# Kernel optimization log

Measured on AMD Instinct MI355X. Metric: run time of the kernel, lower is better.

## Reference

```python
import jax, jax.numpy as jnp
import numpy as np

B, N, T, F, H, O = 32, 256, 64, 16, 128, 1  # batch, nodes, seq_len, input, hidden, output


def setup_inputs() -> dict:
    key = jax.random.key(0)
    ks = jax.random.split(key, 14)
    s = 0.05
    nrm = lambda k, shp: jax.random.normal(k, shp, jnp.float32) * s
    return {
        "x": jax.random.normal(ks[0], (B, N, T, F), jnp.float32),
        "A": jax.random.normal(ks[1], (N, N), jnp.float32),
        "W_ih0": nrm(ks[2], (4 * H, F)),
        "W_hh0": nrm(ks[3], (4 * H, H)),
        "b_ih0": nrm(ks[4], (4 * H,)),
        "b_hh0": nrm(ks[5], (4 * H,)),
        "W_ih1": nrm(ks[6], (4 * H, H)),
        "W_hh1": nrm(ks[7], (4 * H, H)),
        "b_ih1": nrm(ks[8], (4 * H,)),
        "b_hh1": nrm(ks[9], (4 * H,)),
        "W1": nrm(ks[10], (H, H)),
        "W2": nrm(ks[11], (H, H)),
        "W3": nrm(ks[12], (H, H)),
        "Wfc": nrm(ks[13], (O, H)),
    }


def _lstm_layer(inp, W_ih, W_hh, b_ih, b_hh):
    # inp: (BN, T, F_in). PyTorch LSTM gate order: i, f, g, o.
    BN = inp.shape[0]
    Hd = W_hh.shape[1]
    h0 = jnp.zeros((BN, Hd), inp.dtype)
    c0 = jnp.zeros((BN, Hd), inp.dtype)

    def step(carry, x_t):
        h, c = carry
        g = x_t @ W_ih.T + b_ih + h @ W_hh.T + b_hh
        i, f, gg, o = jnp.split(g, 4, axis=-1)
        c = jax.nn.sigmoid(f) * c + jax.nn.sigmoid(i) * jnp.tanh(gg)
        h = jax.nn.sigmoid(o) * jnp.tanh(c)
        return (h, c), h

    (hT, _), hs = jax.lax.scan(step, (h0, c0), jnp.swapaxes(inp, 0, 1))
    return jnp.swapaxes(hs, 0, 1), hT  # (BN, T, H), (BN, H)


def reference(x, A, W_ih0, W_hh0, b_ih0, b_hh0, W_ih1, W_hh1, b_ih1, b_hh1, W1, W2, W3, Wfc):
    Bx, Nx, Tx, Fx = x.shape
    # Batch the per-node LSTM calls: all (batch, node) pairs share LSTM weights.
    xs = x.reshape(Bx * Nx, Tx, Fx)
    h1_seq, _ = _lstm_layer(xs, W_ih0, W_hh0, b_ih0, b_hh0)
    _, hT = _lstm_layer(h1_seq, W_ih1, W_hh1, b_ih1, b_hh1)  # last layer final hidden
    h_LSTM = hT.reshape(Bx, Nx, -1).transpose(0, 2, 1)  # (B, H, N)

    A_p = jax.nn.sigmoid(A)
    HA = jnp.einsum('bhn,nl->bhl', h_LSTM, A_p)        # H @ A'
    h_A = HA.transpose(0, 2, 1)                        # (B, N, H)
    W1hA = jnp.einsum('bnh,gh->bgn', h_A, W1)          # (B, H, N)
    mid = jax.nn.relu(jnp.einsum('bnh,gh->bng', h_A, W2))
    W3r = jnp.einsum('bng,fg->bfn', mid, W3)           # (B, H, N)
    ATW = jnp.einsum('bhn,nl->bhl', W3r, A_p)
    alpha = 0.9
    h_out = (1.0 - alpha) * ATW + alpha * W1hA         # (B, H, N)
    # Per-node MLP (shared weights) + sigmoid, batched over nodes.
    out = jax.nn.sigmoid(jnp.einsum('bhn,oh->bno', h_out, Wfc))  # (B, N, O)
    return out
```

## Files before the change

### kernel.cpp

```cpp
#include <hip/hip_runtime.h>


typedef __attribute__((ext_vector_type(4))) float f32x4;
typedef __attribute__((ext_vector_type(2))) float f32x2;
typedef __attribute__((ext_vector_type(8))) __bf16 bf16x8;
typedef __attribute__((ext_vector_type(8))) unsigned short u16x8;
typedef __attribute__((ext_vector_type(4))) unsigned short u16x4;

#define DEV static __device__ __forceinline__

DEV unsigned short f2bf(float f) {
  unsigned u = __builtin_bit_cast(unsigned, f);
  u = u + 0x7fffu + ((u >> 16) & 1u);
  return (unsigned short)(u >> 16);
}
DEV float bf2f(unsigned short s) {
  unsigned u = ((unsigned)s) << 16;
  return __builtin_bit_cast(float, u);
}

DEV float fexp2(float x) { return __builtin_amdgcn_exp2f(x); }
DEV f32x2 exp2v2(f32x2 x) { f32x2 r; r[0] = fexp2(x[0]); r[1] = fexp2(x[1]); return r; }
DEV f32x2 rcpv2(f32x2 x) {
  f32x2 r; r[0] = __builtin_amdgcn_rcpf(x[0]); r[1] = __builtin_amdgcn_rcpf(x[1]); return r;
}

DEV unsigned cell_pair(f32x2 gi, f32x2 gf, f32x2 gg, f32x2 go, f32x2& cs) {
  const float K2 = 2.88539008f;
  f32x2 one = {1.f, 1.f};
  f32x2 t1 = exp2v2(gg);
  f32x2 t2 = exp2v2((f32x2){-gi[0], -gi[1]});
  f32x2 ef = exp2v2((f32x2){-gf[0], -gf[1]});
  f32x2 d1 = t1 + one;
  f32x2 den1 = d1 * t2 + d1;
  f32x2 it = (t1 - one) * rcpv2(den1);
  cs = rcpv2(one + ef) * cs + (f32x2){K2 * it[0], K2 * it[1]};
  f32x2 t3 = exp2v2(cs);
  f32x2 t4 = exp2v2((f32x2){-go[0], -go[1]});
  f32x2 d3 = t3 + one;
  f32x2 den3 = d3 * t4 + d3;
  f32x2 h = (t3 - one) * rcpv2(den3);
  unsigned r;
  asm("v_cvt_pk_bf16_f32 %0, %1, %2" : "=v"(r) : "v"(h[0]), "v"(h[1]));
  return r;
}

#define O_W0PK   0
#define O_W1PK   163840
#define O_APK    425984
#define O_W1APK  557056
#define O_W2APK  589824
#define O_W3APK  622592
#define O_BIAS0  655360
#define O_BIAS1  657408
#define O_HTT    659456
#define O_HAT    2756608
#define O_MIDT   4853760
#define O_W1HAT  6950912
#define O_W3R    9048064
#define O_XPK    11145216
#define O_H1     44699648

#define PREP_TOT 328704

DEV int gr_unit(int rtg, int lql) { return 16 * (rtg >> 2) + 4 * lql + (rtg & 3); }

__global__ void prep_kernel(const float* __restrict__ A,
    const float* __restrict__ Wih0, const float* __restrict__ Whh0,
    const float* __restrict__ bih0, const float* __restrict__ bhh0,
    const float* __restrict__ Wih1, const float* __restrict__ Whh1,
    const float* __restrict__ bih1, const float* __restrict__ bhh1,
    const float* __restrict__ W1, const float* __restrict__ W2,
    const float* __restrict__ W3, char* __restrict__ ws)
{
  const float K1 = 1.44269504f, K2 = 2.88539008f;
  int idx = blockIdx.x * blockDim.x + threadIdx.x;
  if (idx >= PREP_TOT) return;
  if (idx < 81920) {
    int o = idx, i = o & 7, l = (o >> 3) & 63, f = o >> 9;
    int kt = f % 5, rtg = f / 5;
    int lr = l & 15, lq = l >> 4;
    int p = lr & 3, lql = (lr >> 2) & 3;
    int gc = p * 128 + gr_unit(rtg, lql);
    float sc = (p == 2) ? K2 : K1;
    float v;
    if (kt < 4) v = Whh0[gc * 128 + 32 * kt + 8 * lq + i];
    else {
      int kk = 8 * lq + i;
      v = (kk < 16) ? Wih0[gc * 16 + kk]
                    : (kk == 16 ? (bih0[gc] + bhh0[gc]) : 0.f);
    }
    ((unsigned short*)(ws + O_W0PK))[idx] = f2bf(v * sc);
  } else if (idx < 212992) {
    int o = idx - 81920, i = o & 7, l = (o >> 3) & 63, f = o >> 9;
    int kt = f & 7, rtg = f >> 3;
    int lr = l & 15, lq = l >> 4;
    int p = lr & 3, lql = (lr >> 2) & 3;
    int gc = p * 128 + gr_unit(rtg, lql);
    float sc = (p == 2) ? K2 : K1;
    float v = (kt < 4) ? Wih1[gc * 128 + 32 * kt + 8 * lq + i]
                       : Whh1[gc * 128 + 32 * (kt - 4) + 8 * lq + i];
    ((unsigned short*)(ws + O_W1PK))[o] = f2bf(v * sc);
  } else if (idx < 278528) {
    int o = idx - 212992, i = o & 7, l = (o >> 3) & 63, f = o >> 9;
    int kt = f & 7, ct = f >> 3;
    int n = 32 * kt + 8 * (l >> 4) + i;
    int lc = 16 * ct + (l & 15);
    float e = fexp2(-K1 * A[n * 256 + lc]);
    ((unsigned short*)(ws + O_APK))[o] = f2bf(__builtin_amdgcn_rcpf(1.f + e));
  } else if (idx < 327680) {
    int o = idx - 278528;
    int m = o >> 14;
    int oo = o & 16383;
    int i = oo & 7, l = (oo >> 3) & 63, f = oo >> 9;
    int kt = f & 3, rt = f >> 2;
    int g = 16 * rt + (l & 15);
    int k = 32 * kt + 8 * (l >> 4) + i;
    const float* W = (m == 0) ? W1 : (m == 1) ? W2 : W3;
    unsigned short* dst = (unsigned short*)(ws + ((m == 0) ? O_W1APK : (m == 1) ? O_W2APK : O_W3APK));
    dst[oo] = f2bf(W[g * 128 + k]);
  } else if (idx < 328192) {
    int c = idx - 327680;
    ((float*)(ws + O_BIAS0))[c] = bih0[c] + bhh0[c];
  } else {
    int c = idx - 328192;
    float sc = ((c >> 7) == 2) ? K2 : K1;
    ((float*)(ws + O_BIAS1))[c] = (bih1[c] + bhh1[c]) * sc;
  }
}

__global__ void prepx_kernel(const float* __restrict__ x, char* __restrict__ ws)
{
  int tid = blockIdx.x * 256 + threadIdx.x;
  int dat = (tid < 1048576) ? 1 : 0;
  int id = tid & 1048575;
  int half = id & 1, t = (id >> 1) & 63, row = id >> 7;
  u16x8 v = (u16x8)0;
  if (dat) {
    const float* p = x + ((long)row * 64 + t) * 16 + 8 * half;
    float4 a = *(const float4*)p;
    float4 b = *(const float4*)(p + 4);
    v[0] = f2bf(a.x); v[1] = f2bf(a.y); v[2] = f2bf(a.z); v[3] = f2bf(a.w);
    v[4] = f2bf(b.x); v[5] = f2bf(b.y); v[6] = f2bf(b.z); v[7] = f2bf(b.w);
  } else if (half == 0) {
    v[0] = 0x3F80;
  }
  int lane = (dat ? 0 : 32) + half * 16 + (row & 15);
  int rt = row >> 4;
  ((u16x8*)(ws + O_XPK))[(rt * 64 + t) * 64 + lane] = v;
}

__global__ __launch_bounds__(512, 2) void lstm0_k(char* __restrict__ ws, int row_base)
{
  const unsigned short* W0pk = (const unsigned short*)(ws + O_W0PK);
  const unsigned short* xpk = (const unsigned short*)(ws + O_XPK);
  unsigned short* h1 = (unsigned short*)(ws + O_H1);

  int tid = threadIdx.x;
  int Wv = tid >> 6, l = tid & 63, lr = l & 15, lq = l >> 4;
  int lrow = blockIdx.x * 16;
  long grow0 = (long)row_base + lrow;

  __shared__ unsigned char hlds[2][4096];
  ((unsigned long long*)hlds[0])[tid] = 0ull;

  bf16x8 Af[4][5];
#pragma unroll
  for (int rt = 0; rt < 4; rt++)
#pragma unroll
    for (int kt = 0; kt < 5; kt++)
      Af[rt][kt] = ((const bf16x8*)W0pk)[((4 * Wv + rt) * 5 + kt) * 64 + l];

  f32x2 cs01 = {0.f, 0.f}, cs23 = {0.f, 0.f};

  int rd[4];
#pragma unroll
  for (int kt = 0; kt < 4; kt++)
    rd[kt] = lr * 256 + ((64 * kt + 16 * lq) ^ ((lr & 7) << 4));
  int whp = lr * 256 + ((32 * Wv + 8 * lq) ^ ((lr & 7) << 4));

  int pr = tid >> 5, pc2 = tid & 31;
  int sld = pr * 256 + ((8 * pc2) ^ ((pr & 7) << 4));
  unsigned short* st = h1 + (long)(lrow + pr) * 8192 + 4 * pc2;

  const bf16x8* xp = (const bf16x8*)xpk + (grow0 >> 4) * 4096 + l;
  bf16x8 xb = xp[0];
  __syncthreads();

  for (int t = 0; t < 64; t++) {
    const unsigned char* rbuf = hlds[t & 1];
    unsigned char* wbuf = hlds[(t & 1) ^ 1];
    int tn = (t < 63) ? t + 1 : 63;
    bf16x8 xbn = xp[tn * 64];

    f32x4 acc[4];
#pragma unroll
    for (int rt = 0; rt < 4; rt++) acc[rt] = (f32x4){0.f, 0.f, 0.f, 0.f};
#pragma unroll
    for (int kt = 0; kt < 4; kt++) {
      bf16x8 hb = *(const bf16x8*)(rbuf + rd[kt]);
#pragma unroll
      for (int rt = 0; rt < 4; rt++)
        acc[rt] = __builtin_amdgcn_mfma_f32_16x16x32_bf16(Af[rt][kt], hb, acc[rt], 0, 0, 0);
    }
#pragma unroll
    for (int rt = 0; rt < 4; rt++)
      acc[rt] = __builtin_amdgcn_mfma_f32_16x16x32_bf16(Af[rt][4], xb, acc[rt], 0, 0, 0);

    unsigned pk01 = cell_pair((f32x2){acc[0][0], acc[1][0]}, (f32x2){acc[0][1], acc[1][1]},
                              (f32x2){acc[0][2], acc[1][2]}, (f32x2){acc[0][3], acc[1][3]}, cs01);
    unsigned pk23 = cell_pair((f32x2){acc[2][0], acc[3][0]}, (f32x2){acc[2][1], acc[3][1]},
                              (f32x2){acc[2][2], acc[3][2]}, (f32x2){acc[2][3], acc[3][3]}, cs23);
    unsigned long long pk = ((unsigned long long)pk23 << 32) | pk01;
    *(unsigned long long*)(wbuf + whp) = pk;
    xb = xbn;
    __syncthreads();
    *(unsigned long long*)(st + t * 128) =
        *(const unsigned long long*)(hlds[(t & 1) ^ 1] + sld);
  }
}

__global__ __launch_bounds__(512, 2) void lstm1_k(char* __restrict__ ws, int row_base)
{
  const unsigned short* W1pk = (const unsigned short*)(ws + O_W1PK);
  const float* bias1 = (const float*)(ws + O_BIAS1);
  const unsigned short* h1 = (const unsigned short*)(ws + O_H1);
  unsigned short* hTt = (unsigned short*)(ws + O_HTT);

  int tid = threadIdx.x;
  int Wv = tid >> 6, l = tid & 63, lr = l & 15, lq = l >> 4;
  int lrow = blockIdx.x * 16;
  long grow0 = (long)row_base + lrow;

  __shared__ unsigned char hlds[2][4096];
  __shared__ unsigned char h1s[2][4096];
  ((unsigned long long*)hlds[0])[tid] = 0ull;

  int prow = tid >> 5, pc2 = tid & 31;
  const unsigned short* s0 = h1 + (long)(lrow + prow) * 8192 + 4 * pc2;
  int d0 = prow * 256 + ((8 * pc2) ^ ((prow & 7) << 4));
  *(unsigned long long*)(h1s[0] + d0) = *(const unsigned long long*)s0;

  bf16x8 Af[4][8];
#pragma unroll
  for (int rt = 0; rt < 4; rt++)
#pragma unroll
    for (int kt = 0; kt < 8; kt++)
      Af[rt][kt] = ((const bf16x8*)W1pk)[((4 * Wv + rt) * 8 + kt) * 64 + l];

  f32x4 bias_c[4];
#pragma unroll
  for (int rt = 0; rt < 4; rt++)
#pragma unroll
    for (int r = 0; r < 4; r++)
      bias_c[rt][r] = bias1[r * 128 + 16 * Wv + 4 * lq + rt];

  f32x2 cs01 = {0.f, 0.f}, cs23 = {0.f, 0.f};

  int rd[4];
#pragma unroll
  for (int kt = 0; kt < 4; kt++)
    rd[kt] = lr * 256 + ((64 * kt + 16 * lq) ^ ((lr & 7) << 4));
  int whp = lr * 256 + ((32 * Wv + 8 * lq) ^ ((lr & 7) << 4));
  __syncthreads();

  for (int t = 0; t < 64; t++) {
    const unsigned char* rbuf = hlds[t & 1];
    unsigned char* wbuf = hlds[(t & 1) ^ 1];
    const unsigned char* h1r = h1s[t & 1];
    unsigned char* h1w = h1s[(t & 1) ^ 1];
    int tn = (t < 63) ? t + 1 : 63;
    unsigned long long pf = *(const unsigned long long*)(s0 + tn * 128);

    f32x4 acc[4];
#pragma unroll
    for (int rt = 0; rt < 4; rt++) acc[rt] = bias_c[rt];
#pragma unroll
    for (int kt = 0; kt < 4; kt++) {
      bf16x8 xb = *(const bf16x8*)(h1r + rd[kt]);
#pragma unroll
      for (int rt = 0; rt < 4; rt++)
        acc[rt] = __builtin_amdgcn_mfma_f32_16x16x32_bf16(Af[rt][kt], xb, acc[rt], 0, 0, 0);
    }
#pragma unroll
    for (int kt = 0; kt < 4; kt++) {
      bf16x8 hb = *(const bf16x8*)(rbuf + rd[kt]);
#pragma unroll
      for (int rt = 0; rt < 4; rt++)
        acc[rt] = __builtin_amdgcn_mfma_f32_16x16x32_bf16(Af[rt][4 + kt], hb, acc[rt], 0, 0, 0);
    }
    unsigned pk01 = cell_pair((f32x2){acc[0][0], acc[1][0]}, (f32x2){acc[0][1], acc[1][1]},
                              (f32x2){acc[0][2], acc[1][2]}, (f32x2){acc[0][3], acc[1][3]}, cs01);
    unsigned pk23 = cell_pair((f32x2){acc[2][0], acc[3][0]}, (f32x2){acc[2][1], acc[3][1]},
                              (f32x2){acc[2][2], acc[3][2]}, (f32x2){acc[2][3], acc[3][3]}, cs23);
    *(unsigned long long*)(wbuf + whp) = ((unsigned long long)pk23 << 32) | pk01;
    *(unsigned long long*)(h1w + d0) = pf;
    __syncthreads();
  }

  {
    unsigned long long hp = *(const unsigned long long*)(hlds[0] + whp);
    long grow = grow0 + lr;
    long base = ((grow >> 8) * 128) * 256 + (grow & 255);
    int u0 = 16 * Wv + 4 * lq;
#pragma unroll
    for (int j = 0; j < 4; j++)
      hTt[base + (long)(u0 + j) * 256] = (unsigned short)((hp >> (16 * j)) & 0xffff);
  }
}

__global__ __launch_bounds__(256, 2) void g1_kernel(char* __restrict__ ws)
{
  const unsigned short* hTt = (const unsigned short*)(ws + O_HTT);
  const unsigned short* Apk = (const unsigned short*)(ws + O_APK);
  unsigned short* HAt = (unsigned short*)(ws + O_HAT);
  int tid = threadIdx.x, w = tid >> 6, l = tid & 63, lr = l & 15, lq = l >> 4;
  int bi = blockIdx.x;
  int b = bi >> 3, rtp = (bi >> 1) & 3, ch = bi & 1;
  f32x4 acc[2][2];
#pragma unroll
  for (int i = 0; i < 2; i++)
#pragma unroll
    for (int j = 0; j < 2; j++) acc[i][j] = (f32x4){0.f, 0.f, 0.f, 0.f};
  for (int kt = 0; kt < 8; kt++) {
    bf16x8 af[2];
#pragma unroll
    for (int rtl = 0; rtl < 2; rtl++) {
      int rt = rtp * 2 + rtl;
      af[rtl] = *(const bf16x8*)(hTt + (long)(b * 128 + 16 * rt + lr) * 256 + 32 * kt + 8 * lq);
    }
#pragma unroll
    for (int cti = 0; cti < 2; cti++) {
      int ct = w * 4 + ch * 2 + cti;
      bf16x8 bf = ((const bf16x8*)Apk)[(ct * 8 + kt) * 64 + l];
#pragma unroll
      for (int rtl = 0; rtl < 2; rtl++)
        acc[rtl][cti] = __builtin_amdgcn_mfma_f32_16x16x32_bf16(af[rtl], bf, acc[rtl][cti], 0, 0, 0);
    }
  }
#pragma unroll
  for (int rtl = 0; rtl < 2; rtl++)
#pragma unroll
    for (int cti = 0; cti < 2; cti++) {
      int rt = rtp * 2 + rtl, ct = w * 4 + ch * 2 + cti;
      u16x4 pk;
#pragma unroll
      for (int r = 0; r < 4; r++) pk[r] = f2bf(acc[rtl][cti][r]);
      *(u16x4*)(HAt + (long)(b * 256 + 16 * ct + lr) * 128 + 16 * rt + 4 * lq) = pk;
    }
}

__global__ __launch_bounds__(256, 2) void g2_kernel(char* __restrict__ ws)
{
  const unsigned short* HAt = (const unsigned short*)(ws + O_HAT);
  const unsigned short* W1apk = (const unsigned short*)(ws + O_W1APK);
  const unsigned short* W2apk = (const unsigned short*)(ws + O_W2APK);
  unsigned short* W1hAt = (unsigned short*)(ws + O_W1HAT);
  unsigned short* midT = (unsigned short*)(ws + O_MIDT);
  int tid = threadIdx.x, w = tid >> 6, l = tid & 63, lr = l & 15, lq = l >> 4;
  int bi = blockIdx.x;
  int b = bi >> 3, rtp = (bi >> 1) & 3, ch = bi & 1;
  f32x4 a1[2][2], a2[2][2];
#pragma unroll
  for (int i = 0; i < 2; i++)
#pragma unroll
    for (int j = 0; j < 2; j++) { a1[i][j] = (f32x4){0.f,0.f,0.f,0.f}; a2[i][j] = (f32x4){0.f,0.f,0.f,0.f}; }
  for (int kt = 0; kt < 4; kt++) {
    bf16x8 af1[2], af2[2];
#pragma unroll
    for (int rtl = 0; rtl < 2; rtl++) {
      int rt = rtp * 2 + rtl;
      af1[rtl] = ((const bf16x8*)W1apk)[(rt * 4 + kt) * 64 + l];
      af2[rtl] = ((const bf16x8*)W2apk)[(rt * 4 + kt) * 64 + l];
    }
#pragma unroll
    for (int cti = 0; cti < 2; cti++) {
      int ct = w * 4 + ch * 2 + cti;
      bf16x8 bf = *(const bf16x8*)(HAt + (long)(b * 256 + 16 * ct + lr) * 128 + 32 * kt + 8 * lq);
#pragma unroll
      for (int rtl = 0; rtl < 2; rtl++) {
        a1[rtl][cti] = __builtin_amdgcn_mfma_f32_16x16x32_bf16(af1[rtl], bf, a1[rtl][cti], 0, 0, 0);
        a2[rtl][cti] = __builtin_amdgcn_mfma_f32_16x16x32_bf16(af2[rtl], bf, a2[rtl][cti], 0, 0, 0);
      }
    }
  }
#pragma unroll
  for (int rtl = 0; rtl < 2; rtl++)
#pragma unroll
    for (int cti = 0; cti < 2; cti++) {
      int rt = rtp * 2 + rtl, ct = w * 4 + ch * 2 + cti;
      u16x4 p1, p2;
#pragma unroll
      for (int r = 0; r < 4; r++) {
        p1[r] = f2bf(a1[rtl][cti][r]);
        p2[r] = f2bf(fmaxf(a2[rtl][cti][r], 0.f));
      }
      long off = (long)(b * 256 + 16 * ct + lr) * 128 + 16 * rt + 4 * lq;
      *(u16x4*)(W1hAt + off) = p1;
      *(u16x4*)(midT + off) = p2;
    }
}

__global__ __launch_bounds__(256, 2) void g3_kernel(char* __restrict__ ws)
{
  const unsigned short* midT = (const unsigned short*)(ws + O_MIDT);
  const unsigned short* W3apk = (const unsigned short*)(ws + O_W3APK);
  unsigned short* W3r = (unsigned short*)(ws + O_W3R);
  int tid = threadIdx.x, w = tid >> 6, l = tid & 63, lr = l & 15, lq = l >> 4;
  int bi = blockIdx.x;
  int b = bi >> 3, rtp = (bi >> 1) & 3, ch = bi & 1;
  f32x4 acc[2][2];
#pragma unroll
  for (int i = 0; i < 2; i++)
#pragma unroll
    for (int j = 0; j < 2; j++) acc[i][j] = (f32x4){0.f, 0.f, 0.f, 0.f};
  for (int kt = 0; kt < 4; kt++) {
    bf16x8 af[2];
#pragma unroll
    for (int rtl = 0; rtl < 2; rtl++)
      af[rtl] = ((const bf16x8*)W3apk)[((rtp * 2 + rtl) * 4 + kt) * 64 + l];
#pragma unroll
    for (int cti = 0; cti < 2; cti++) {
      int ct = w * 4 + ch * 2 + cti;
      bf16x8 bf = *(const bf16x8*)(midT + (long)(b * 256 + 16 * ct + lr) * 128 + 32 * kt + 8 * lq);
#pragma unroll
      for (int rtl = 0; rtl < 2; rtl++)
        acc[rtl][cti] = __builtin_amdgcn_mfma_f32_16x16x32_bf16(af[rtl], bf, acc[rtl][cti], 0, 0, 0);
    }
  }
#pragma unroll
  for (int rtl = 0; rtl < 2; rtl++)
#pragma unroll
    for (int cti = 0; cti < 2; cti++) {
      int rt = rtp * 2 + rtl, ct = w * 4 + ch * 2 + cti;
#pragma unroll
      for (int r = 0; r < 4; r++)
        W3r[(long)(b * 128 + 16 * rt + 4 * lq + r) * 256 + 16 * ct + lr] = f2bf(acc[rtl][cti][r]);
    }
}

__global__ __launch_bounds__(256, 2) void g4_kernel(char* __restrict__ ws,
    const float* __restrict__ Wfc, float* __restrict__ out)
{
  const unsigned short* W3r = (const unsigned short*)(ws + O_W3R);
  const unsigned short* Apk = (const unsigned short*)(ws + O_APK);
  const unsigned short* W1hAt = (const unsigned short*)(ws + O_W1HAT);
  int tid = threadIdx.x, w = tid >> 6, l = tid & 63, lr = l & 15, lq = l >> 4;
  int bi = blockIdx.x;
  int b = bi >> 2, cq = bi & 3;
  int ct = cq * 4 + w;
  f32x4 acc[8];
#pragma unroll
  for (int i = 0; i < 8; i++) acc[i] = (f32x4){0.f, 0.f, 0.f, 0.f};
  for (int kt = 0; kt < 8; kt++) {
    bf16x8 bfv = ((const bf16x8*)Apk)[(ct * 8 + kt) * 64 + l];
#pragma unroll
    for (int rt = 0; rt < 8; rt++) {
      bf16x8 af = *(const bf16x8*)(W3r + (long)(b * 128 + 16 * rt + lr) * 256 + 32 * kt + 8 * lq);
      acc[rt] = __builtin_amdgcn_mfma_f32_16x16x32_bf16(af, bfv, acc[rt], 0, 0, 0);
    }
  }
  float psum = 0.f;
#pragma unroll
  for (int rt = 0; rt < 8; rt++) {
    float4 wf = *(const float4*)(Wfc + 16 * rt + 4 * lq);
    u16x4 wv = *(const u16x4*)(W1hAt + (long)(b * 256 + 16 * ct + lr) * 128 + 16 * rt + 4 * lq);
    psum += wf.x * (0.1f * acc[rt][0] + 0.9f * bf2f(wv[0]));
    psum += wf.y * (0.1f * acc[rt][1] + 0.9f * bf2f(wv[1]));
    psum += wf.z * (0.1f * acc[rt][2] + 0.9f * bf2f(wv[2]));
    psum += wf.w * (0.1f * acc[rt][3] + 0.9f * bf2f(wv[3]));
  }
  psum += __shfl_xor(psum, 16);
  psum += __shfl_xor(psum, 32);
  if (lq == 0) out[b * 256 + ct * 16 + lr] = __builtin_amdgcn_rcpf(1.f + fexp2(-1.44269504f * psum));
}

extern "C" void kernel_launch(void* const* d_in, const int* in_sizes, int n_in,
                              void* d_out, int out_size, void* d_ws, size_t ws_size,
                              hipStream_t stream)
{
  const float* x    = (const float*)d_in[0];
  const float* A    = (const float*)d_in[1];
  const float* Wih0 = (const float*)d_in[2];
  const float* Whh0 = (const float*)d_in[3];
  const float* bih0 = (const float*)d_in[4];
  const float* bhh0 = (const float*)d_in[5];
  const float* Wih1 = (const float*)d_in[6];
  const float* Whh1 = (const float*)d_in[7];
  const float* bih1 = (const float*)d_in[8];
  const float* bhh1 = (const float*)d_in[9];
  const float* W1   = (const float*)d_in[10];
  const float* W2   = (const float*)d_in[11];
  const float* W3   = (const float*)d_in[12];
  const float* Wfc  = (const float*)d_in[13];
  char* ws = (char*)d_ws;

  prep_kernel<<<(PREP_TOT + 255) / 256, 256, 0, stream>>>(
      A, Wih0, Whh0, bih0, bhh0, Wih1, Whh1, bih1, bhh1, W1, W2, W3, ws);
  prepx_kernel<<<8192, 256, 0, stream>>>(x, ws);

  size_t need_full = (size_t)O_H1 + 134217728u;
  size_t need_half = (size_t)O_H1 + 67108864u;
  if (ws_size >= need_full) {
    lstm0_k<<<512, 512, 0, stream>>>(ws, 0);
    lstm1_k<<<512, 512, 0, stream>>>(ws, 0);
  } else if (ws_size >= need_half) {
    for (int c = 0; c < 2; c++) {
      lstm0_k<<<256, 512, 0, stream>>>(ws, c * 4096);
      lstm1_k<<<256, 512, 0, stream>>>(ws, c * 4096);
    }
  } else {
    for (int c = 0; c < 4; c++) {
      lstm0_k<<<128, 512, 0, stream>>>(ws, c * 2048);
      lstm1_k<<<128, 512, 0, stream>>>(ws, c * 2048);
    }
  }

  g1_kernel<<<256, 256, 0, stream>>>(ws);
  g2_kernel<<<256, 256, 0, stream>>>(ws);
  g3_kernel<<<256, 256, 0, stream>>>(ws);
  g4_kernel<<<128, 256, 0, stream>>>(ws, Wfc, (float*)d_out);
}
```

Measured before the change: 269.8 us.

## Switch LSTM recurrence to 32x32x16 MFMA with 32-row blocks of 1024 threads

Both LSTM kernels move from 16x16x32 MFMAs with four row tiles per wave to a single 32x32x16 MFMA accumulator per wave. Each block now handles 32 sequence rows with 16 waves, so weights, LDS layouts, swizzles and the x packing are reorganised to match. s_setprio is raised around the MFMA chain. The aim is fewer MFMA issues and more rows per block, at the cost of larger LDS buffers and a larger block, which may limit occupancy under launch_bounds(1024,4).

```diff
diff --git a/kernel.cpp b/kernel.cpp
--- a/kernel.cpp
+++ b/kernel.cpp
@@ -2,6 +2,7 @@
 
 
 typedef __attribute__((ext_vector_type(4))) float f32x4;
+typedef __attribute__((ext_vector_type(16))) float f32x16;
 typedef __attribute__((ext_vector_type(2))) float f32x2;
 typedef __attribute__((ext_vector_type(8))) __bf16 bf16x8;
 typedef __attribute__((ext_vector_type(8))) unsigned short u16x8;
@@ -63,8 +64,6 @@
 
 #define PREP_TOT 328704
 
-DEV int gr_unit(int rtg, int lql) { return 16 * (rtg >> 2) + 4 * lql + (rtg & 3); }
-
 __global__ void prep_kernel(const float* __restrict__ A,
     const float* __restrict__ Wih0, const float* __restrict__ Whh0,
     const float* __restrict__ bih0, const float* __restrict__ bhh0,
@@ -78,28 +77,29 @@
   if (idx >= PREP_TOT) return;
   if (idx < 81920) {
     int o = idx, i = o & 7, l = (o >> 3) & 63, f = o >> 9;
-    int kt = f % 5, rtg = f / 5;
-    int lr = l & 15, lq = l >> 4;
-    int p = lr & 3, lql = (lr >> 2) & 3;
-    int gc = p * 128 + gr_unit(rtg, lql);
+    int kt = f % 10, W = f / 10;
+    int rho = l & 31, hik = l >> 5;
+    int p = rho & 3, hi = (rho >> 2) & 1, q = rho >> 3;
+    int gc = p * 128 + 8 * W + 4 * hi + q;
     float sc = (p == 2) ? K2 : K1;
+    int k = 16 * kt + 8 * hik + i;
     float v;
-    if (kt < 4) v = Whh0[gc * 128 + 32 * kt + 8 * lq + i];
+    if (k < 128) v = Whh0[gc * 128 + k];
     else {
-      int kk = 8 * lq + i;
+      int kk = k - 128;
       v = (kk < 16) ? Wih0[gc * 16 + kk]
                     : (kk == 16 ? (bih0[gc] + bhh0[gc]) : 0.f);
     }
     ((unsigned short*)(ws + O_W0PK))[idx] = f2bf(v * sc);
   } else if (idx < 212992) {
     int o = idx - 81920, i = o & 7, l = (o >> 3) & 63, f = o >> 9;
-    int kt = f & 7, rtg = f >> 3;
-    int lr = l & 15, lq = l >> 4;
-    int p = lr & 3, lql = (lr >> 2) & 3;
-    int gc = p * 128 + gr_unit(rtg, lql);
+    int kt = f & 15, W = f >> 4;
+    int rho = l & 31, hik = l >> 5;
+    int p = rho & 3, hi = (rho >> 2) & 1, q = rho >> 3;
+    int gc = p * 128 + 8 * W + 4 * hi + q;
     float sc = (p == 2) ? K2 : K1;
-    float v = (kt < 4) ? Wih1[gc * 128 + 32 * kt + 8 * lq + i]
-                       : Whh1[gc * 128 + 32 * (kt - 4) + 8 * lq + i];
+    int k = 16 * kt + 8 * hik + i;
+    float v = (k < 128) ? Wih1[gc * 128 + k] : Whh1[gc * 128 + (k - 128)];
     ((unsigned short*)(ws + O_W1PK))[o] = f2bf(v * sc);
   } else if (idx < 278528) {
     int o = idx - 212992, i = o & 7, l = (o >> 3) & 63, f = o >> 9;
@@ -132,95 +132,92 @@
 __global__ void prepx_kernel(const float* __restrict__ x, char* __restrict__ ws)
 {
   int tid = blockIdx.x * 256 + threadIdx.x;
-  int dat = (tid < 1048576) ? 1 : 0;
-  int id = tid & 1048575;
-  int half = id & 1, t = (id >> 1) & 63, row = id >> 7;
+  int lane = tid & 63;
+  int slice = (tid >> 6) & 1;
+  int t = (tid >> 7) & 63;
+  int rt32 = tid >> 13;
+  int col = lane & 31, hi = lane >> 5;
   u16x8 v = (u16x8)0;
-  if (dat) {
-    const float* p = x + ((long)row * 64 + t) * 16 + 8 * half;
+  if (slice == 0) {
+    const float* p = x + ((long)(rt32 * 32 + col) * 64 + t) * 16 + 8 * hi;
     float4 a = *(const float4*)p;
     float4 b = *(const float4*)(p + 4);
     v[0] = f2bf(a.x); v[1] = f2bf(a.y); v[2] = f2bf(a.z); v[3] = f2bf(a.w);
     v[4] = f2bf(b.x); v[5] = f2bf(b.y); v[6] = f2bf(b.z); v[7] = f2bf(b.w);
-  } else if (half == 0) {
+  } else if (hi == 0) {
     v[0] = 0x3F80;
   }
-  int lane = (dat ? 0 : 32) + half * 16 + (row & 15);
-  int rt = row >> 4;
-  ((u16x8*)(ws + O_XPK))[(rt * 64 + t) * 64 + lane] = v;
-}
-
-__global__ __launch_bounds__(512, 2) void lstm0_k(char* __restrict__ ws, int row_base)
+  ((u16x8*)(ws + O_XPK))[tid] = v;
+}
+
+__global__ __launch_bounds__(1024, 4) void lstm0_k(char* __restrict__ ws, int row_base)
 {
   const unsigned short* W0pk = (const unsigned short*)(ws + O_W0PK);
   const unsigned short* xpk = (const unsigned short*)(ws + O_XPK);
   unsigned short* h1 = (unsigned short*)(ws + O_H1);
 
   int tid = threadIdx.x;
-  int Wv = tid >> 6, l = tid & 63, lr = l & 15, lq = l >> 4;
-  int lrow = blockIdx.x * 16;
+  int Wv = tid >> 6, l = tid & 63, col = l & 31, hi = l >> 5;
+  int lrow = blockIdx.x * 32;
   long grow0 = (long)row_base + lrow;
 
-  __shared__ unsigned char hlds[2][4096];
+  __shared__ unsigned char hlds[2][8192];
   ((unsigned long long*)hlds[0])[tid] = 0ull;
 
-  bf16x8 Af[4][5];
-#pragma unroll
-  for (int rt = 0; rt < 4; rt++)
-#pragma unroll
-    for (int kt = 0; kt < 5; kt++)
-      Af[rt][kt] = ((const bf16x8*)W0pk)[((4 * Wv + rt) * 5 + kt) * 64 + l];
+  bf16x8 Af[10];
+#pragma unroll
+  for (int kt = 0; kt < 10; kt++)
+    Af[kt] = ((const bf16x8*)W0pk)[(Wv * 10 + kt) * 64 + l];
 
   f32x2 cs01 = {0.f, 0.f}, cs23 = {0.f, 0.f};
 
-  int rd[4];
-#pragma unroll
-  for (int kt = 0; kt < 4; kt++)
-    rd[kt] = lr * 256 + ((64 * kt + 16 * lq) ^ ((lr & 7) << 4));
-  int whp = lr * 256 + ((32 * Wv + 8 * lq) ^ ((lr & 7) << 4));
-
-  int pr = tid >> 5, pc2 = tid & 31;
-  int sld = pr * 256 + ((8 * pc2) ^ ((pr & 7) << 4));
-  unsigned short* st = h1 + (long)(lrow + pr) * 8192 + 4 * pc2;
-
-  const bf16x8* xp = (const bf16x8*)xpk + (grow0 >> 4) * 4096 + l;
-  bf16x8 xb = xp[0];
+  int rd[8];
+#pragma unroll
+  for (int ks = 0; ks < 8; ks++)
+    rd[ks] = col * 256 + ((32 * ks + 16 * hi) ^ ((col & 15) << 4));
+  int whp = col * 256 + ((16 * Wv + 8 * hi) ^ ((col & 15) << 4));
+
+  int pr = tid >> 5, pc8 = tid & 31;
+  int sld = pr * 256 + ((8 * pc8) ^ ((pr & 15) << 4));
+  unsigned short* st = h1 + (long)(lrow + pr) * 8192 + 4 * pc8;
+
+  long xbase = (grow0 >> 5) * 8192 + l;
+  const bf16x8* xpf = (const bf16x8*)xpk;
+  bf16x8 xb0 = xpf[xbase], xb1 = xpf[xbase + 64];
   __syncthreads();
 
   for (int t = 0; t < 64; t++) {
     const unsigned char* rbuf = hlds[t & 1];
     unsigned char* wbuf = hlds[(t & 1) ^ 1];
     int tn = (t < 63) ? t + 1 : 63;
-    bf16x8 xbn = xp[tn * 64];
-
-    f32x4 acc[4];
-#pragma unroll
-    for (int rt = 0; rt < 4; rt++) acc[rt] = (f32x4){0.f, 0.f, 0.f, 0.f};
-#pragma unroll
-    for (int kt = 0; kt < 4; kt++) {
-      bf16x8 hb = *(const bf16x8*)(rbuf + rd[kt]);
-#pragma unroll
-      for (int rt = 0; rt < 4; rt++)
-        acc[rt] = __builtin_amdgcn_mfma_f32_16x16x32_bf16(Af[rt][kt], hb, acc[rt], 0, 0, 0);
-    }
-#pragma unroll
-    for (int rt = 0; rt < 4; rt++)
-      acc[rt] = __builtin_amdgcn_mfma_f32_16x16x32_bf16(Af[rt][4], xb, acc[rt], 0, 0, 0);
-
-    unsigned pk01 = cell_pair((f32x2){acc[0][0], acc[1][0]}, (f32x2){acc[0][1], acc[1][1]},
-                              (f32x2){acc[0][2], acc[1][2]}, (f32x2){acc[0][3], acc[1][3]}, cs01);
-    unsigned pk23 = cell_pair((f32x2){acc[2][0], acc[3][0]}, (f32x2){acc[2][1], acc[3][1]},
-                              (f32x2){acc[2][2], acc[3][2]}, (f32x2){acc[2][3], acc[3][3]}, cs23);
-    unsigned long long pk = ((unsigned long long)pk23 << 32) | pk01;
-    *(unsigned long long*)(wbuf + whp) = pk;
-    xb = xbn;
+    bf16x8 xb0n = xpf[xbase + tn * 128];
+    bf16x8 xb1n = xpf[xbase + tn * 128 + 64];
+
+    f32x16 acc = (f32x16)0.f;
+    __builtin_amdgcn_s_setprio(1);
+#pragma unroll
+    for (int ks = 0; ks < 8; ks++) {
+      bf16x8 hb = *(const bf16x8*)(rbuf + rd[ks]);
+      acc = __builtin_amdgcn_mfma_f32_32x32x16_bf16(Af[ks], hb, acc, 0, 0, 0);
+    }
+    acc = __builtin_amdgcn_mfma_f32_32x32x16_bf16(Af[8], xb0, acc, 0, 0, 0);
+    acc = __builtin_amdgcn_mfma_f32_32x32x16_bf16(Af[9], xb1, acc, 0, 0, 0);
+    __builtin_amdgcn_s_setprio(0);
+
+    unsigned pk01 = cell_pair((f32x2){acc[0], acc[4]}, (f32x2){acc[1], acc[5]},
+                              (f32x2){acc[2], acc[6]}, (f32x2){acc[3], acc[7]}, cs01);
+    unsigned pk23 = cell_pair((f32x2){acc[8], acc[12]}, (f32x2){acc[9], acc[13]},
+                              (f32x2){acc[10], acc[14]}, (f32x2){acc[11], acc[15]}, cs23);
+    *(unsigned long long*)(wbuf + whp) =
+        ((unsigned long long)pk23 << 32) | pk01;
+    xb0 = xb0n; xb1 = xb1n;
     __syncthreads();
     *(unsigned long long*)(st + t * 128) =
         *(const unsigned long long*)(hlds[(t & 1) ^ 1] + sld);
   }
 }
 
-__global__ __launch_bounds__(512, 2) void lstm1_k(char* __restrict__ ws, int row_base)
+__global__ __launch_bounds__(1024, 4) void lstm1_k(char* __restrict__ ws, int row_base)
 {
   const unsigned short* W1pk = (const unsigned short*)(ws + O_W1PK);
   const float* bias1 = (const float*)(ws + O_BIAS1);
@@ -228,40 +225,37 @@
   unsigned short* hTt = (unsigned short*)(ws + O_HTT);
 
   int tid = threadIdx.x;
-  int Wv = tid >> 6, l = tid & 63, lr = l & 15, lq = l >> 4;
-  int lrow = blockIdx.x * 16;
+  int Wv = tid >> 6, l = tid & 63, col = l & 31, hi = l >> 5;
+  int lrow = blockIdx.x * 32;
   long grow0 = (long)row_base + lrow;
 
-  __shared__ unsigned char hlds[2][4096];
-  __shared__ unsigned char h1s[2][4096];
+  __shared__ unsigned char hlds[2][8192];
+  __shared__ unsigned char h1s[2][8192];
   ((unsigned long long*)hlds[0])[tid] = 0ull;
 
-  int prow = tid >> 5, pc2 = tid & 31;
-  const unsigned short* s0 = h1 + (long)(lrow + prow) * 8192 + 4 * pc2;
-  int d0 = prow * 256 + ((8 * pc2) ^ ((prow & 7) << 4));
+  int prow = tid >> 5, pc8 = tid & 31;
+  const unsigned short* s0 = h1 + (long)(lrow + prow) * 8192 + 4 * pc8;
+  int d0 = prow * 256 + ((8 * pc8) ^ ((prow & 15) << 4));
   *(unsigned long long*)(h1s[0] + d0) = *(const unsigned long long*)s0;
 
-  bf16x8 Af[4][8];
-#pragma unroll
-  for (int rt = 0; rt < 4; rt++)
-#pragma unroll
-    for (int kt = 0; kt < 8; kt++)
-      Af[rt][kt] = ((const bf16x8*)W1pk)[((4 * Wv + rt) * 8 + kt) * 64 + l];
-
-  f32x4 bias_c[4];
-#pragma unroll
-  for (int rt = 0; rt < 4; rt++)
-#pragma unroll
-    for (int r = 0; r < 4; r++)
-      bias_c[rt][r] = bias1[r * 128 + 16 * Wv + 4 * lq + rt];
+  bf16x8 Af[16];
+#pragma unroll
+  for (int kt = 0; kt < 16; kt++)
+    Af[kt] = ((const bf16x8*)W1pk)[(Wv * 16 + kt) * 64 + l];
+
+  int u0 = 8 * Wv + 4 * hi;
+  f32x16 bias_c;
+#pragma unroll
+  for (int r = 0; r < 16; r++)
+    bias_c[r] = bias1[(r & 3) * 128 + u0 + (r >> 2)];
 
   f32x2 cs01 = {0.f, 0.f}, cs23 = {0.f, 0.f};
 
-  int rd[4];
-#pragma unroll
-  for (int kt = 0; kt < 4; kt++)
-    rd[kt] = lr * 256 + ((64 * kt + 16 * lq) ^ ((lr & 7) << 4));
-  int whp = lr * 256 + ((32 * Wv + 8 * lq) ^ ((lr & 7) << 4));
+  int rd[8];
+#pragma unroll
+  for (int ks = 0; ks < 8; ks++)
+    rd[ks] = col * 256 + ((32 * ks + 16 * hi) ^ ((col & 15) << 4));
+  int whp = col * 256 + ((16 * Wv + 8 * hi) ^ ((col & 15) << 4));
   __syncthreads();
 
   for (int t = 0; t < 64; t++) {
@@ -272,37 +266,34 @@
     int tn = (t < 63) ? t + 1 : 63;
     unsigned long long pf = *(const unsigned long long*)(s0 + tn * 128);
 
-    f32x4 acc[4];
-#pragma unroll
-    for (int rt = 0; rt < 4; rt++) acc[rt] = bias_c[rt];
-#pragma unroll
-    for (int kt = 0; kt < 4; kt++) {
-      bf16x8 xb = *(const bf16x8*)(h1r + rd[kt]);
-#pragma unroll
-      for (int rt = 0; rt < 4; rt++)
-        acc[rt] = __builtin_amdgcn_mfma_f32_16x16x32_bf16(Af[rt][kt], xb, acc[rt], 0, 0, 0);
-    }
-#pragma unroll
-    for (int kt = 0; kt < 4; kt++) {
-      bf16x8 hb = *(const bf16x8*)(rbuf + rd[kt]);
-#pragma unroll
-      for (int rt = 0; rt < 4; rt++)
-        acc[rt] = __builtin_amdgcn_mfma_f32_16x16x32_bf16(Af[rt][4 + kt], hb, acc[rt], 0, 0, 0);
-    }
-    unsigned pk01 = cell_pair((f32x2){acc[0][0], acc[1][0]}, (f32x2){acc[0][1], acc[1][1]},
-                              (f32x2){acc[0][2], acc[1][2]}, (f32x2){acc[0][3], acc[1][3]}, cs01);
-    unsigned pk23 = cell_pair((f32x2){acc[2][0], acc[3][0]}, (f32x2){acc[2][1], acc[3][1]},
-                              (f32x2){acc[2][2], acc[3][2]}, (f32x2){acc[2][3], acc[3][3]}, cs23);
-    *(unsigned long long*)(wbuf + whp) = ((unsigned long long)pk23 << 32) | pk01;
+    f32x16 acc = bias_c;
+    __builtin_amdgcn_s_setprio(1);
+#pragma unroll
+    for (int ks = 0; ks < 8; ks++) {
+      bf16x8 xb = *(const bf16x8*)(h1r + rd[ks]);
+      acc = __builtin_amdgcn_mfma_f32_32x32x16_bf16(Af[ks], xb, acc, 0, 0, 0);
+    }
+#pragma unroll
+    for (int ks = 0; ks < 8; ks++) {
+      bf16x8 hb = *(const bf16x8*)(rbuf + rd[ks]);
+      acc = __builtin_amdgcn_mfma_f32_32x32x16_bf16(Af[8 + ks], hb, acc, 0, 0, 0);
+    }
+    __builtin_amdgcn_s_setprio(0);
+
+    unsigned pk01 = cell_pair((f32x2){acc[0], acc[4]}, (f32x2){acc[1], acc[5]},
+                              (f32x2){acc[2], acc[6]}, (f32x2){acc[3], acc[7]}, cs01);
+    unsigned pk23 = cell_pair((f32x2){acc[8], acc[12]}, (f32x2){acc[9], acc[13]},
+                              (f32x2){acc[10], acc[14]}, (f32x2){acc[11], acc[15]}, cs23);
+    *(unsigned long long*)(wbuf + whp) =
+        ((unsigned long long)pk23 << 32) | pk01;
     *(unsigned long long*)(h1w + d0) = pf;
     __syncthreads();
   }
 
   {
     unsigned long long hp = *(const unsigned long long*)(hlds[0] + whp);
-    long grow = grow0 + lr;
+    long grow = grow0 + col;
     long base = ((grow >> 8) * 128) * 256 + (grow & 255);
-    int u0 = 16 * Wv + 4 * lq;
 #pragma unroll
     for (int j = 0; j < 4; j++)
       hTt[base + (long)(u0 + j) * 256] = (unsigned short)((hp >> (16 * j)) & 0xffff);
@@ -502,17 +493,17 @@
   size_t need_full = (size_t)O_H1 + 134217728u;
   size_t need_half = (size_t)O_H1 + 67108864u;
   if (ws_size >= need_full) {
-    lstm0_k<<<512, 512, 0, stream>>>(ws, 0);
-    lstm1_k<<<512, 512, 0, stream>>>(ws, 0);
+    lstm0_k<<<256, 1024, 0, stream>>>(ws, 0);
+    lstm1_k<<<256, 1024, 0, stream>>>(ws, 0);
   } else if (ws_size >= need_half) {
     for (int c = 0; c < 2; c++) {
-      lstm0_k<<<256, 512, 0, stream>>>(ws, c * 4096);
-      lstm1_k<<<256, 512, 0, stream>>>(ws, c * 4096);
+      lstm0_k<<<128, 1024, 0, stream>>>(ws, c * 4096);
+      lstm1_k<<<128, 1024, 0, stream>>>(ws, c * 4096);
     }
   } else {
     for (int c = 0; c < 4; c++) {
-      lstm0_k<<<128, 512, 0, stream>>>(ws, c * 2048);
-      lstm1_k<<<128, 512, 0, stream>>>(ws, c * 2048);
+      lstm0_k<<<64, 1024, 0, stream>>>(ws, c * 2048);
+      lstm1_k<<<64, 1024, 0, stream>>>(ws, c * 2048);
     }
   }
 
```

Result: no change. 274.2 us (+1.7%).
